# Optimization experiments

Hardware: AMD Instinct MI355X
Metric: run time of the kernel (lower is better)

## Reference

```python
import jax, jax.numpy as jnp
import numpy as np

N_NODES = 100000
N_EDGES = 1600000
IN_DIM = 128
HID = 64
OUT_DIM = 64


def setup_inputs() -> dict:
    key = jax.random.key(0)
    k = jax.random.split(key, 6)
    x = jax.random.normal(k[0], (N_NODES, IN_DIM), dtype=jnp.float32)
    edge_index = jax.random.randint(k[1], (2, N_EDGES), 0, N_NODES, dtype=jnp.int32)
    W_lin = jax.random.normal(k[2], (HID, IN_DIM), dtype=jnp.float32) * (1.0 / np.sqrt(IN_DIM))
    att = jax.random.uniform(k[3], (2 * HID,), dtype=jnp.float32, minval=-0.1, maxval=0.1)
    W_out = jax.random.normal(k[4], (OUT_DIM, HID), dtype=jnp.float32) * (1.0 / np.sqrt(HID))
    b_out = jax.random.normal(k[5], (OUT_DIM,), dtype=jnp.float32) * 0.01
    return {"x": x, "edge_index": edge_index, "W_lin": W_lin, "att": att, "W_out": W_out, "b_out": b_out}


def reference(x, edge_index, W_lin, att, W_out, b_out):
    n = x.shape[0]
    hid = W_lin.shape[0]
    h = x @ W_lin.T                                   # [N, H]
    # cat([hs,hd])*att summed == (h@a_src)[src] + (h@a_dst)[dst]
    s_node = h @ att[:hid]                            # [N]
    d_node = h @ att[hid:]                            # [N]
    src, dst = edge_index[0], edge_index[1]
    e = jax.nn.leaky_relu(s_node[src] + d_node[dst], negative_slope=0.2)  # [E]
    exp_e = jnp.exp(e - jnp.max(e))                   # global-max stabilized, as in source
    denom = jax.ops.segment_sum(exp_e, dst, num_segments=n)               # [N]
    alpha = exp_e / (denom[dst] + 1e-9)               # [E]
    msg = h[src] * alpha[:, None]                     # [E, H]
    agg = jax.ops.segment_sum(msg, dst, num_segments=n)                   # [N, H]
    z = jax.nn.relu(agg)                              # dropout is identity in eval
    return z @ W_out.T + b_out
```

## Files before the change

### kernel.cpp

```cpp
#include <hip/hip_runtime.h>

#define N_NODES 100000
#define N_EDGES 1600000
#define IN_DIM 128
#define HID 64
#define OUT_DIM 64

typedef __attribute__((ext_vector_type(8))) short short8;
typedef __attribute__((ext_vector_type(4))) float f32x4;
union FragU { short8 v; unsigned u[4]; };

__device__ __forceinline__ unsigned bf16r(float f) {
    unsigned u = __float_as_uint(f);
    return (u + 0x7FFFu + ((u >> 16) & 1u)) >> 16;
}
__device__ __forceinline__ float blo(unsigned u) { return __uint_as_float(u << 16); }
__device__ __forceinline__ float bhi(unsigned u) { return __uint_as_float(u & 0xFFFF0000u); }

#define K1_BLOCKS 1563
#define NB 782
#define CAP 2432
#define P1_BLOCKS 391
#define P1_EPB 4096
#define GRID_TOTAL (K1_BLOCKS + P1_BLOCKS)

__global__ __launch_bounds__(256) void k1_p1(const float* __restrict__ x,
                                             const float* __restrict__ W,
                                             const float* __restrict__ att,
                                             uint4* __restrict__ h4,
                                             float* __restrict__ s,
                                             float* __restrict__ d,
                                             const int* __restrict__ ei,
                                             int* __restrict__ gcount,
                                             unsigned* __restrict__ ibuf) {
    __shared__ float wsL[IN_DIM], wdL[IN_DIM];
    __shared__ __align__(16) unsigned char shmem[4 * 64 * 17 * 4];
    const int tid = threadIdx.x;
    const int bx = blockIdx.x;
    const bool is_p1 = ((bx % 5) == 4) || (bx == GRID_TOTAL - 1);

    if (is_p1) {
        int* cnt  = (int*)shmem;
        int* base = cnt + NB;
        const int blk = (bx == GRID_TOTAL - 1) ? (P1_BLOCKS - 1) : (bx / 5);
        const int e4base = blk * (P1_EPB / 4);
        for (int i = tid; i < NB; i += 256) cnt[i] = 0;
        __syncthreads();
        int pk[4][4];
#pragma unroll
        for (int c = 0; c < 4; ++c) {
            int i4 = e4base + c * 256 + tid;
            if (i4 < N_EDGES / 4) {
                int4 dv = ((const int4*)(ei + N_EDGES))[i4];
                pk[c][0] = dv.x | (atomicAdd(&cnt[dv.x >> 7], 1) << 17);
                pk[c][1] = dv.y | (atomicAdd(&cnt[dv.y >> 7], 1) << 17);
                pk[c][2] = dv.z | (atomicAdd(&cnt[dv.z >> 7], 1) << 17);
                pk[c][3] = dv.w | (atomicAdd(&cnt[dv.w >> 7], 1) << 17);
            }
        }
        __syncthreads();
        for (int b = tid; b < NB; b += 256) {
            int c = cnt[b];
            base[b] = c ? atomicAdd(&gcount[b], c) : 0;
        }
        __syncthreads();
#pragma unroll
        for (int c = 0; c < 4; ++c) {
            int i4 = e4base + c * 256 + tid;
            if (i4 < N_EDGES / 4) {
                int4 sv = ((const int4*)ei)[i4];
                int srcs[4] = {sv.x, sv.y, sv.z, sv.w};
#pragma unroll
                for (int j = 0; j < 4; ++j) {
                    unsigned p   = (unsigned)pk[c][j];
                    unsigned dst = p & 0x1FFFFu;
                    unsigned r   = p >> 17;
                    unsigned bk  = dst >> 7;
                    ibuf[bk * CAP + (unsigned)base[bk] + r] =
                        (unsigned)srcs[j] | ((dst & 127u) << 20);
                }
            }
        }
        return;
    }
    const int kb = bx - (bx + 1) / 5;

    uint4* wlds = (uint4*)shmem;
    if (tid < IN_DIM) {
        float as = 0.f, ad = 0.f;
#pragma unroll
        for (int c = 0; c < HID; ++c) {
            float w = W[c * IN_DIM + tid];
            as += w * att[c];
            ad += w * att[HID + c];
        }
        wsL[tid] = as; wdL[tid] = ad;
    }
    for (int i = tid; i < 1024; i += 256) {
        int ln = i & 63, ks = (i >> 6) & 3, t = i >> 8;
        int fl16 = ln & 15, fq = ln >> 4;
        const float* wp = &W[(t * 16 + fl16) * IN_DIM + ks * 32 + fq * 8];
        float4 wa = *(const float4*)wp;
        float4 wb = *(const float4*)(wp + 4);
        uint4 o;
        o.x = bf16r(wa.x) | (bf16r(wa.y) << 16);
        o.y = bf16r(wa.z) | (bf16r(wa.w) << 16);
        o.z = bf16r(wb.x) | (bf16r(wb.y) << 16);
        o.w = bf16r(wb.z) | (bf16r(wb.w) << 16);
        wlds[i] = o;
    }
    __syncthreads();

    const int lane = tid & 63;
    const int wv = tid >> 6;
    const int l16 = lane & 15;
    const int quad = lane >> 4;
    const int tile = kb * 4 + wv;
    const bool valid = (tile < N_NODES / 16);
    const int rowbase = tile * 16;

    f32x4 acc[4] = {{0.f,0.f,0.f,0.f},{0.f,0.f,0.f,0.f},
                    {0.f,0.f,0.f,0.f},{0.f,0.f,0.f,0.f}};
    float ps = 0.f, pd = 0.f;
    if (valid) {
        const float* xrow = &x[(size_t)(rowbase + l16) * IN_DIM];
#pragma unroll
        for (int ks = 0; ks < 4; ++ks) {
            const int k0 = ks * 32 + quad * 8;
            float4 xa = *(const float4*)&xrow[k0];
            float4 xb = *(const float4*)&xrow[k0 + 4];
            ps += xa.x * wsL[k0]     + xa.y * wsL[k0 + 1]
                + xa.z * wsL[k0 + 2] + xa.w * wsL[k0 + 3]
                + xb.x * wsL[k0 + 4] + xb.y * wsL[k0 + 5]
                + xb.z * wsL[k0 + 6] + xb.w * wsL[k0 + 7];
            pd += xa.x * wdL[k0]     + xa.y * wdL[k0 + 1]
                + xa.z * wdL[k0 + 2] + xa.w * wdL[k0 + 3]
                + xb.x * wdL[k0 + 4] + xb.y * wdL[k0 + 5]
                + xb.z * wdL[k0 + 6] + xb.w * wdL[k0 + 7];
            FragU af;
            af.u[0] = bf16r(xa.x) | (bf16r(xa.y) << 16);
            af.u[1] = bf16r(xa.z) | (bf16r(xa.w) << 16);
            af.u[2] = bf16r(xb.x) | (bf16r(xb.y) << 16);
            af.u[3] = bf16r(xb.z) | (bf16r(xb.w) << 16);
#pragma unroll
            for (int t = 0; t < 4; ++t) {
                FragU bf;
                *(uint4*)&bf = wlds[(t * 4 + ks) * 64 + lane];
                acc[t] = __builtin_amdgcn_mfma_f32_16x16x32_bf16(
                    af.v, bf.v, acc[t], 0, 0, 0);
            }
        }
        ps += __shfl_xor(ps, 16, 64); ps += __shfl_xor(ps, 32, 64);
        pd += __shfl_xor(pd, 16, 64); pd += __shfl_xor(pd, 32, 64);
        if (quad == 0) { s[rowbase + l16] = ps; d[rowbase + l16] = pd; }
    }
    __syncthreads();

    if (valid) {
        float* sc = (float*)shmem + wv * 64 * 17;
#pragma unroll
        for (int t = 0; t < 4; ++t)
#pragma unroll
            for (int r = 0; r < 4; ++r)
                sc[(l16 + 16 * t) * 17 + quad * 4 + r] = acc[t][r];
#pragma unroll
        for (int i = 0; i < 2; ++i) {
            int idx = i * 64 + lane;
            int nrow = idx >> 3, q = idx & 7;
            float v0 = sc[(q * 8 + 0) * 17 + nrow];
            float v1 = sc[(q * 8 + 1) * 17 + nrow];
            float v2 = sc[(q * 8 + 2) * 17 + nrow];
            float v3 = sc[(q * 8 + 3) * 17 + nrow];
            float v4 = sc[(q * 8 + 4) * 17 + nrow];
            float v5 = sc[(q * 8 + 5) * 17 + nrow];
            float v6 = sc[(q * 8 + 6) * 17 + nrow];
            float v7 = sc[(q * 8 + 7) * 17 + nrow];
            uint4 o;
            o.x = bf16r(v0) | (bf16r(v1) << 16);
            o.y = bf16r(v2) | (bf16r(v3) << 16);
            o.z = bf16r(v4) | (bf16r(v5) << 16);
            o.w = bf16r(v6) | (bf16r(v7) << 16);
            h4[(size_t)(rowbase + nrow) * 8 + q] = o;
        }
    }
}

__global__ __launch_bounds__(512) void k_sort_agg(const unsigned* __restrict__ ibuf,
                                                  const int* __restrict__ gcount,
                                                  const float* __restrict__ s,
                                                  const float* __restrict__ d,
                                                  const uint4* __restrict__ h4,
                                                  uint4* __restrict__ zp) {
    __shared__ uint2 el[CAP];
    __shared__ int cnt2[128], off2[128];
    __shared__ float dloc[128];
    __shared__ int wred[2];
    const int tid  = threadIdx.x;
    const int lane = tid & 63;
    const int wv   = tid >> 6;
    const int b    = blockIdx.x;

    if (tid < 128) {
        cnt2[tid] = 0;
        int dn = b * 128 + tid;
        dloc[tid] = (dn < N_NODES) ? d[dn] : 0.f;
    }
    __syncthreads();
    const int count = gcount[b];

    unsigned vk[5];
    int rk_[5];
#pragma unroll
    for (int ki = 0; ki < 5; ++ki) {
        int k = tid + ki * 512;
        vk[ki] = 0u; rk_[ki] = -1;
        if (k < count) {
            unsigned v = ibuf[(size_t)b * CAP + k];
            int dl = (int)(v >> 20);
            rk_[ki] = atomicAdd(&cnt2[dl], 1);
            vk[ki] = v;
        }
    }
    __syncthreads();

    int v0 = 0, sc0 = 0;
    if (tid < 128) {
        v0 = cnt2[tid];
        sc0 = v0;
#pragma unroll
        for (int off = 1; off < 64; off <<= 1) {
            int t = __shfl_up(sc0, off, 64);
            if (lane >= off) sc0 += t;
        }
        if (lane == 63) wred[wv] = sc0;
    }
    __syncthreads();
    if (tid < 128) {
        int excl = sc0 - v0 + ((wv == 1) ? wred[0] : 0);
        off2[tid] = excl;
    }
    __syncthreads();

#pragma unroll
    for (int ki = 0; ki < 5; ++ki) {
        if (rk_[ki] >= 0) {
            unsigned v = vk[ki];
            unsigned src = v & 0xFFFFFu;
            int dl = (int)(v >> 20);
            float e = s[src] + dloc[dl];
            e = (e > 0.f) ? e : 0.2f * e;
            float ex = __expf(e);
            el[off2[dl] + rk_[ki]] = make_uint2(src, __float_as_uint(ex));
        }
    }
    __syncthreads();

    const int l8 = tid & 7;
    const int g = tid >> 3;
#pragma unroll
    for (int half = 0; half < 2; ++half) {
        const int dl = g + half * 64;
        const int node = b * 128 + dl;
        if (node < N_NODES) {
            const int o = off2[dl];
            const int n = cnt2[dl];
            float a0 = 0.f, a1 = 0.f, a2 = 0.f, a3 = 0.f;
            float a4 = 0.f, a5 = 0.f, a6 = 0.f, a7 = 0.f, se = 0.f;
            int j = 0;
            for (; j + 7 < n; j += 8) {
                uint2 r0 = el[o + j];
                uint2 r1 = el[o + j + 1];
                uint2 r2 = el[o + j + 2];
                uint2 r3 = el[o + j + 3];
                uint2 r4 = el[o + j + 4];
                uint2 r5 = el[o + j + 5];
                uint2 r6 = el[o + j + 6];
                uint2 r7 = el[o + j + 7];
                uint4 g0 = h4[(size_t)r0.x * 8u + l8];
                uint4 g1 = h4[(size_t)r1.x * 8u + l8];
                uint4 g2 = h4[(size_t)r2.x * 8u + l8];
                uint4 g3 = h4[(size_t)r3.x * 8u + l8];
                uint4 g4 = h4[(size_t)r4.x * 8u + l8];
                uint4 g5 = h4[(size_t)r5.x * 8u + l8];
                uint4 g6 = h4[(size_t)r6.x * 8u + l8];
                uint4 g7 = h4[(size_t)r7.x * 8u + l8];
                float e0 = __uint_as_float(r0.y), e1 = __uint_as_float(r1.y);
                float e2 = __uint_as_float(r2.y), e3 = __uint_as_float(r3.y);
                float e4 = __uint_as_float(r4.y), e5 = __uint_as_float(r5.y);
                float e6 = __uint_as_float(r6.y), e7 = __uint_as_float(r7.y);
                se += ((e0 + e1) + (e2 + e3)) + ((e4 + e5) + (e6 + e7));
                a0 += e0 * blo(g0.x) + e1 * blo(g1.x) + e2 * blo(g2.x) + e3 * blo(g3.x)
                    + e4 * blo(g4.x) + e5 * blo(g5.x) + e6 * blo(g6.x) + e7 * blo(g7.x);
                a1 += e0 * bhi(g0.x) + e1 * bhi(g1.x) + e2 * bhi(g2.x) + e3 * bhi(g3.x)
                    + e4 * bhi(g4.x) + e5 * bhi(g5.x) + e6 * bhi(g6.x) + e7 * bhi(g7.x);
                a2 += e0 * blo(g0.y) + e1 * blo(g1.y) + e2 * blo(g2.y) + e3 * blo(g3.y)
                    + e4 * blo(g4.y) + e5 * blo(g5.y) + e6 * blo(g6.y) + e7 * blo(g7.y);
                a3 += e0 * bhi(g0.y) + e1 * bhi(g1.y) + e2 * bhi(g2.y) + e3 * bhi(g3.y)
                    + e4 * bhi(g4.y) + e5 * bhi(g5.y) + e6 * bhi(g6.y) + e7 * bhi(g7.y);
                a4 += e0 * blo(g0.z) + e1 * blo(g1.z) + e2 * blo(g2.z) + e3 * blo(g3.z)
                    + e4 * blo(g4.z) + e5 * blo(g5.z) + e6 * blo(g6.z) + e7 * blo(g7.z);
                a5 += e0 * bhi(g0.z) + e1 * bhi(g1.z) + e2 * bhi(g2.z) + e3 * bhi(g3.z)
                    + e4 * bhi(g4.z) + e5 * bhi(g5.z) + e6 * bhi(g6.z) + e7 * bhi(g7.z);
                a6 += e0 * blo(g0.w) + e1 * blo(g1.w) + e2 * blo(g2.w) + e3 * blo(g3.w)
                    + e4 * blo(g4.w) + e5 * blo(g5.w) + e6 * blo(g6.w) + e7 * blo(g7.w);
                a7 += e0 * bhi(g0.w) + e1 * bhi(g1.w) + e2 * bhi(g2.w) + e3 * bhi(g3.w)
                    + e4 * bhi(g4.w) + e5 * bhi(g5.w) + e6 * bhi(g6.w) + e7 * bhi(g7.w);
            }
            if (j + 3 < n) {
                uint2 r0 = el[o + j];
                uint2 r1 = el[o + j + 1];
                uint2 r2 = el[o + j + 2];
                uint2 r3 = el[o + j + 3];
                uint4 g0 = h4[(size_t)r0.x * 8u + l8];
                uint4 g1 = h4[(size_t)r1.x * 8u + l8];
                uint4 g2 = h4[(size_t)r2.x * 8u + l8];
                uint4 g3 = h4[(size_t)r3.x * 8u + l8];
                float e0 = __uint_as_float(r0.y), e1 = __uint_as_float(r1.y);
                float e2 = __uint_as_float(r2.y), e3 = __uint_as_float(r3.y);
                se += (e0 + e1) + (e2 + e3);
                a0 += e0 * blo(g0.x) + e1 * blo(g1.x) + e2 * blo(g2.x) + e3 * blo(g3.x);
                a1 += e0 * bhi(g0.x) + e1 * bhi(g1.x) + e2 * bhi(g2.x) + e3 * bhi(g3.x);
                a2 += e0 * blo(g0.y) + e1 * blo(g1.y) + e2 * blo(g2.y) + e3 * blo(g3.y);
                a3 += e0 * bhi(g0.y) + e1 * bhi(g1.y) + e2 * bhi(g2.y) + e3 * bhi(g3.y);
                a4 += e0 * blo(g0.z) + e1 * blo(g1.z) + e2 * blo(g2.z) + e3 * blo(g3.z);
                a5 += e0 * bhi(g0.z) + e1 * bhi(g1.z) + e2 * bhi(g2.z) + e3 * bhi(g3.z);
                a6 += e0 * blo(g0.w) + e1 * blo(g1.w) + e2 * blo(g2.w) + e3 * blo(g3.w);
                a7 += e0 * bhi(g0.w) + e1 * bhi(g1.w) + e2 * bhi(g2.w) + e3 * bhi(g3.w);
                j += 4;
            }
            for (; j < n; ++j) {
                uint2 r = el[o + j];
                uint4 gg = h4[(size_t)r.x * 8u + l8];
                float e = __uint_as_float(r.y);
                se += e;
                a0 += e * blo(gg.x); a1 += e * bhi(gg.x);
                a2 += e * blo(gg.y); a3 += e * bhi(gg.y);
                a4 += e * blo(gg.z); a5 += e * bhi(gg.z);
                a6 += e * blo(gg.w); a7 += e * bhi(gg.w);
            }
            float inv = 1.f / (se + 1e-9f);
            uint4 o4;
            o4.x = bf16r(fmaxf(a0 * inv, 0.f)) | (bf16r(fmaxf(a1 * inv, 0.f)) << 16);
            o4.y = bf16r(fmaxf(a2 * inv, 0.f)) | (bf16r(fmaxf(a3 * inv, 0.f)) << 16);
            o4.z = bf16r(fmaxf(a4 * inv, 0.f)) | (bf16r(fmaxf(a5 * inv, 0.f)) << 16);
            o4.w = bf16r(fmaxf(a6 * inv, 0.f)) | (bf16r(fmaxf(a7 * inv, 0.f)) << 16);
            zp[(size_t)node * 8 + l8] = o4;
        }
    }
}

#define K4_M 128
#define ZPAD 132
#define WPAD4 68

__global__ __launch_bounds__(256) void k4_out(const uint2* __restrict__ zp2,
                                              const float* __restrict__ W_out,
                                              const float* __restrict__ b_out,
                                              float* __restrict__ out) {
    __shared__ float zsT[HID * ZPAD];
    __shared__ float wsT[HID * WPAD4];
    const int tid = threadIdx.x;
    const int m0g = blockIdx.x * K4_M;
    for (int i = tid; i < OUT_DIM * HID; i += 256) {
        int c = i >> 6, k = i & 63;
        wsT[k * WPAD4 + c] = W_out[i];
    }
    for (int i = tid; i < K4_M * 16; i += 256) {
        int m = i >> 4, q = i & 15;
        int row = m0g + m;
        uint2 v = (row < N_NODES) ? zp2[row * 16 + q] : make_uint2(0u, 0u);
        int kb = q * 4;
        zsT[(kb + 0) * ZPAD + m] = blo(v.x);
        zsT[(kb + 1) * ZPAD + m] = bhi(v.x);
        zsT[(kb + 2) * ZPAD + m] = blo(v.y);
        zsT[(kb + 3) * ZPAD + m] = bhi(v.y);
    }
    __syncthreads();
    const int m0 = (tid & 31) * 4;
    const int c0 = (tid >> 5) * 8;
    float acc[4][8] = {};
#pragma unroll 4
    for (int k = 0; k < HID; ++k) {
        const float4 zv = *(const float4*)&zsT[k * ZPAD + m0];
        const float4 wa = *(const float4*)&wsT[k * WPAD4 + c0];
        const float4 wb = *(const float4*)&wsT[k * WPAD4 + c0 + 4];
#pragma unroll
        for (int i2 = 0; i2 < 4; ++i2) {
            float zi = (&zv.x)[i2];
            acc[i2][0] += zi * wa.x; acc[i2][1] += zi * wa.y;
            acc[i2][2] += zi * wa.z; acc[i2][3] += zi * wa.w;
            acc[i2][4] += zi * wb.x; acc[i2][5] += zi * wb.y;
            acc[i2][6] += zi * wb.z; acc[i2][7] += zi * wb.w;
        }
    }
    const float4 b0 = *(const float4*)&b_out[c0];
    const float4 b1 = *(const float4*)&b_out[c0 + 4];
#pragma unroll
    for (int i2 = 0; i2 < 4; ++i2) {
        int row = m0g + m0 + i2;
        if (row < N_NODES) {
            *(float4*)&out[row * OUT_DIM + c0] =
                make_float4(acc[i2][0] + b0.x, acc[i2][1] + b0.y,
                            acc[i2][2] + b0.z, acc[i2][3] + b0.w);
            *(float4*)&out[row * OUT_DIM + c0 + 4] =
                make_float4(acc[i2][4] + b1.x, acc[i2][5] + b1.y,
                            acc[i2][6] + b1.z, acc[i2][7] + b1.w);
        }
    }
}

extern "C" void kernel_launch(void* const* d_in, const int* in_sizes, int n_in,
                              void* d_out, int out_size, void* d_ws, size_t ws_size,
                              hipStream_t stream) {
    const float* x     = (const float*)d_in[0];
    const int*   ei    = (const int*)d_in[1];
    const float* W_lin = (const float*)d_in[2];
    const float* att   = (const float*)d_in[3];
    const float* W_out = (const float*)d_in[4];
    const float* b_out = (const float*)d_in[5];
    float* out = (float*)d_out;

    char* ws = (char*)d_ws;
    unsigned* h2        = (unsigned*)(ws);
    float*    s         = (float*)(ws + 12800000);
    float*    d         = (float*)(ws + 13200000);
    int*      gcount    = (int*)  (ws + 13600000);
    unsigned* ibuf      = (unsigned*)(ws + 14800016);
    unsigned* zp        = (unsigned*)(ws + 27600016);

    hipMemsetAsync(gcount, 0, NB * sizeof(int), stream);

    k1_p1<<<GRID_TOTAL, 256, 0, stream>>>(
        x, W_lin, att, (uint4*)h2, s, d, ei, gcount, ibuf);
    k_sort_agg<<<NB, 512, 0, stream>>>(ibuf, gcount, s, d, (const uint4*)h2, (uint4*)zp);
    k4_out<<<(N_NODES + K4_M - 1) / K4_M, 256, 0, stream>>>(
        (const uint2*)zp, W_out, b_out, out);
}
```

Measured before the change: 198.1 us.

## Split each 128-node aggregation bucket across two 256-thread blocks

The sort-and-aggregate kernel now launches two 256-thread blocks per 128-destination bucket instead of one 512-thread block. Each block handles 64 destinations and keeps only the edges whose local index falls in its half. The prefix scan becomes a single-wavefront scan and the LDS edge list shrinks, which should let more blocks stay resident and spread work more finely. In exchange, each bucket's edge list is read twice from global memory and each thread holds twice as many candidate registers.

```diff
diff --git a/kernel.cpp b/kernel.cpp
--- a/kernel.cpp
+++ b/kernel.cpp
@@ -20,6 +20,7 @@
 #define K1_BLOCKS 1563
 #define NB 782
 #define CAP 2432
+#define CAP_H 1280
 #define P1_BLOCKS 391
 #define P1_EPB 4096
 #define GRID_TOTAL (K1_BLOCKS + P1_BLOCKS)
@@ -185,68 +186,63 @@
     }
 }
 
-__global__ __launch_bounds__(512) void k_sort_agg(const unsigned* __restrict__ ibuf,
+__global__ __launch_bounds__(256) void k_sort_agg(const unsigned* __restrict__ ibuf,
                                                   const int* __restrict__ gcount,
                                                   const float* __restrict__ s,
                                                   const float* __restrict__ d,
                                                   const uint4* __restrict__ h4,
                                                   uint4* __restrict__ zp) {
-    __shared__ uint2 el[CAP];
-    __shared__ int cnt2[128], off2[128];
-    __shared__ float dloc[128];
-    __shared__ int wred[2];
-    const int tid  = threadIdx.x;
-    const int lane = tid & 63;
-    const int wv   = tid >> 6;
-    const int b    = blockIdx.x;
-
-    if (tid < 128) {
+    __shared__ uint2 el[CAP_H];
+    __shared__ int cnt2[64], off2[64];
+    __shared__ float dloc[64];
+    const int tid    = threadIdx.x;
+    const int bucket = blockIdx.x >> 1;
+    const int halfid = blockIdx.x & 1;
+    const int nodeb  = bucket * 128 + halfid * 64;
+
+    if (tid < 64) {
         cnt2[tid] = 0;
-        int dn = b * 128 + tid;
+        int dn = nodeb + tid;
         dloc[tid] = (dn < N_NODES) ? d[dn] : 0.f;
     }
     __syncthreads();
-    const int count = gcount[b];
-
-    unsigned vk[5];
-    int rk_[5];
-#pragma unroll
-    for (int ki = 0; ki < 5; ++ki) {
-        int k = tid + ki * 512;
+    const int count = gcount[bucket];
+
+    unsigned vk[10];
+    int rk_[10];
+#pragma unroll
+    for (int ki = 0; ki < 10; ++ki) {
+        int k = tid + ki * 256;
         vk[ki] = 0u; rk_[ki] = -1;
         if (k < count) {
-            unsigned v = ibuf[(size_t)b * CAP + k];
+            unsigned v = ibuf[(size_t)bucket * CAP + k];
             int dl = (int)(v >> 20);
-            rk_[ki] = atomicAdd(&cnt2[dl], 1);
-            vk[ki] = v;
-        }
-    }
-    __syncthreads();
-
-    int v0 = 0, sc0 = 0;
-    if (tid < 128) {
-        v0 = cnt2[tid];
-        sc0 = v0;
+            if ((dl >> 6) == halfid) {
+                rk_[ki] = atomicAdd(&cnt2[dl & 63], 1);
+                vk[ki] = v;
+            }
+        }
+    }
+    __syncthreads();
+
+    if (tid < 64) {
+        int v0 = cnt2[tid];
+        int sc0 = v0;
 #pragma unroll
         for (int off = 1; off < 64; off <<= 1) {
             int t = __shfl_up(sc0, off, 64);
-            if (lane >= off) sc0 += t;
-        }
-        if (lane == 63) wred[wv] = sc0;
-    }
-    __syncthreads();
-    if (tid < 128) {
-        int excl = sc0 - v0 + ((wv == 1) ? wred[0] : 0);
-        off2[tid] = excl;
-    }
-    __syncthreads();
-
-#pragma unroll
-    for (int ki = 0; ki < 5; ++ki) {
+            if (tid >= off) sc0 += t;
+        }
+        off2[tid] = sc0 - v0;
+    }
+    __syncthreads();
+
+#pragma unroll
+    for (int ki = 0; ki < 10; ++ki) {
         if (rk_[ki] >= 0) {
             unsigned v = vk[ki];
             unsigned src = v & 0xFFFFFu;
-            int dl = (int)(v >> 20);
+            int dl = (int)(v >> 20) & 63;
             float e = s[src] + dloc[dl];
             e = (e > 0.f) ? e : 0.2f * e;
             float ex = __expf(e);
@@ -259,8 +255,8 @@
     const int g = tid >> 3;
 #pragma unroll
     for (int half = 0; half < 2; ++half) {
-        const int dl = g + half * 64;
-        const int node = b * 128 + dl;
+        const int dl = g + half * 32;
+        const int node = nodeb + dl;
         if (node < N_NODES) {
             const int o = off2[dl];
             const int n = cnt2[dl];
@@ -432,7 +428,7 @@
 
     k1_p1<<<GRID_TOTAL, 256, 0, stream>>>(
         x, W_lin, att, (uint4*)h2, s, d, ei, gcount, ibuf);
-    k_sort_agg<<<NB, 512, 0, stream>>>(ibuf, gcount, s, d, (const uint4*)h2, (uint4*)zp);
+    k_sort_agg<<<2 * NB, 256, 0, stream>>>(ibuf, gcount, s, d, (const uint4*)h2, (uint4*)zp);
     k4_out<<<(N_NODES + K4_M - 1) / K4_M, 256, 0, stream>>>(
         (const uint2*)zp, W_out, b_out, out);
 }
```

New measurement: 199.4 us. Within noise of the previous version (+0.7%).

## Fuse output projection into aggregation kernel using bf16 MFMA

Applied to the files above, without the earlier changes.

Removes the separate output-projection kernel and the global round trip of the bf16 aggregated activations. Each aggregation block stages its 128 relu'd node rows in the shared edge buffer, then computes z @ W_out^T + b_out with 16x16x32 bf16 MFMA instructions, with W_out held as register fragments. This saves one launch plus the zp write and read. In exchange it adds W_out loads and bf16 conversion per block, more register pressure, and W_out is now rounded to bf16 where it was fp32 before.

```diff
diff --git a/kernel.cpp b/kernel.cpp
--- a/kernel.cpp
+++ b/kernel.cpp
@@ -190,21 +190,46 @@
                                                   const float* __restrict__ s,
                                                   const float* __restrict__ d,
                                                   const uint4* __restrict__ h4,
-                                                  uint4* __restrict__ zp) {
-    __shared__ uint2 el[CAP];
+                                                  const float* __restrict__ W_out,
+                                                  const float* __restrict__ b_out,
+                                                  float* __restrict__ out) {
+    __shared__ __align__(16) unsigned char elbuf[CAP * 8];
+    uint2* el    = (uint2*)elbuf;
+    uint4* zloc4 = (uint4*)elbuf;
     __shared__ int cnt2[128], off2[128];
     __shared__ float dloc[128];
     __shared__ int wred[2];
     const int tid  = threadIdx.x;
     const int lane = tid & 63;
     const int wv   = tid >> 6;
+    const int l16  = lane & 15;
+    const int quad = lane >> 4;
     const int b    = blockIdx.x;
+    const int nodeb = b * 128;
 
     if (tid < 128) {
         cnt2[tid] = 0;
-        int dn = b * 128 + tid;
+        int dn = nodeb + tid;
         dloc[tid] = (dn < N_NODES) ? d[dn] : 0.f;
     }
+
+    FragU wfrag[4][2];
+#pragma unroll
+    for (int t = 0; t < 4; ++t)
+#pragma unroll
+        for (int ks = 0; ks < 2; ++ks) {
+            const float* wp = &W_out[(t * 16 + l16) * HID + ks * 32 + quad * 8];
+            float4 wa = *(const float4*)wp;
+            float4 wb = *(const float4*)(wp + 4);
+            wfrag[t][ks].u[0] = bf16r(wa.x) | (bf16r(wa.y) << 16);
+            wfrag[t][ks].u[1] = bf16r(wa.z) | (bf16r(wa.w) << 16);
+            wfrag[t][ks].u[2] = bf16r(wb.x) | (bf16r(wb.y) << 16);
+            wfrag[t][ks].u[3] = bf16r(wb.z) | (bf16r(wb.w) << 16);
+        }
+    float bias[4];
+#pragma unroll
+    for (int t = 0; t < 4; ++t) bias[t] = b_out[t * 16 + l16];
+
     __syncthreads();
     const int count = gcount[b];
 
@@ -257,10 +282,11 @@
 
     const int l8 = tid & 7;
     const int g = tid >> 3;
+    uint4 o4h[2] = {make_uint4(0,0,0,0), make_uint4(0,0,0,0)};
 #pragma unroll
     for (int half = 0; half < 2; ++half) {
         const int dl = g + half * 64;
-        const int node = b * 128 + dl;
+        const int node = nodeb + dl;
         if (node < N_NODES) {
             const int o = off2[dl];
             const int n = cnt2[dl];
@@ -339,72 +365,36 @@
                 a6 += e * blo(gg.w); a7 += e * bhi(gg.w);
             }
             float inv = 1.f / (se + 1e-9f);
-            uint4 o4;
-            o4.x = bf16r(fmaxf(a0 * inv, 0.f)) | (bf16r(fmaxf(a1 * inv, 0.f)) << 16);
-            o4.y = bf16r(fmaxf(a2 * inv, 0.f)) | (bf16r(fmaxf(a3 * inv, 0.f)) << 16);
-            o4.z = bf16r(fmaxf(a4 * inv, 0.f)) | (bf16r(fmaxf(a5 * inv, 0.f)) << 16);
-            o4.w = bf16r(fmaxf(a6 * inv, 0.f)) | (bf16r(fmaxf(a7 * inv, 0.f)) << 16);
-            zp[(size_t)node * 8 + l8] = o4;
-        }
-    }
-}
-
-#define K4_M 128
-#define ZPAD 132
-#define WPAD4 68
-
-__global__ __launch_bounds__(256) void k4_out(const uint2* __restrict__ zp2,
-                                              const float* __restrict__ W_out,
-                                              const float* __restrict__ b_out,
-                                              float* __restrict__ out) {
-    __shared__ float zsT[HID * ZPAD];
-    __shared__ float wsT[HID * WPAD4];
-    const int tid = threadIdx.x;
-    const int m0g = blockIdx.x * K4_M;
-    for (int i = tid; i < OUT_DIM * HID; i += 256) {
-        int c = i >> 6, k = i & 63;
-        wsT[k * WPAD4 + c] = W_out[i];
-    }
-    for (int i = tid; i < K4_M * 16; i += 256) {
-        int m = i >> 4, q = i & 15;
-        int row = m0g + m;
-        uint2 v = (row < N_NODES) ? zp2[row * 16 + q] : make_uint2(0u, 0u);
-        int kb = q * 4;
-        zsT[(kb + 0) * ZPAD + m] = blo(v.x);
-        zsT[(kb + 1) * ZPAD + m] = bhi(v.x);
-        zsT[(kb + 2) * ZPAD + m] = blo(v.y);
-        zsT[(kb + 3) * ZPAD + m] = bhi(v.y);
-    }
-    __syncthreads();
-    const int m0 = (tid & 31) * 4;
-    const int c0 = (tid >> 5) * 8;
-    float acc[4][8] = {};
-#pragma unroll 4
-    for (int k = 0; k < HID; ++k) {
-        const float4 zv = *(const float4*)&zsT[k * ZPAD + m0];
-        const float4 wa = *(const float4*)&wsT[k * WPAD4 + c0];
-        const float4 wb = *(const float4*)&wsT[k * WPAD4 + c0 + 4];
-#pragma unroll
-        for (int i2 = 0; i2 < 4; ++i2) {
-            float zi = (&zv.x)[i2];
-            acc[i2][0] += zi * wa.x; acc[i2][1] += zi * wa.y;
-            acc[i2][2] += zi * wa.z; acc[i2][3] += zi * wa.w;
-            acc[i2][4] += zi * wb.x; acc[i2][5] += zi * wb.y;
-            acc[i2][6] += zi * wb.z; acc[i2][7] += zi * wb.w;
-        }
-    }
-    const float4 b0 = *(const float4*)&b_out[c0];
-    const float4 b1 = *(const float4*)&b_out[c0 + 4];
-#pragma unroll
-    for (int i2 = 0; i2 < 4; ++i2) {
-        int row = m0g + m0 + i2;
-        if (row < N_NODES) {
-            *(float4*)&out[row * OUT_DIM + c0] =
-                make_float4(acc[i2][0] + b0.x, acc[i2][1] + b0.y,
-                            acc[i2][2] + b0.z, acc[i2][3] + b0.w);
-            *(float4*)&out[row * OUT_DIM + c0 + 4] =
-                make_float4(acc[i2][4] + b1.x, acc[i2][5] + b1.y,
-                            acc[i2][6] + b1.z, acc[i2][7] + b1.w);
+            o4h[half].x = bf16r(fmaxf(a0 * inv, 0.f)) | (bf16r(fmaxf(a1 * inv, 0.f)) << 16);
+            o4h[half].y = bf16r(fmaxf(a2 * inv, 0.f)) | (bf16r(fmaxf(a3 * inv, 0.f)) << 16);
+            o4h[half].z = bf16r(fmaxf(a4 * inv, 0.f)) | (bf16r(fmaxf(a5 * inv, 0.f)) << 16);
+            o4h[half].w = bf16r(fmaxf(a6 * inv, 0.f)) | (bf16r(fmaxf(a7 * inv, 0.f)) << 16);
+        }
+    }
+    __syncthreads();
+
+    zloc4[(size_t)g * 9 + l8] = o4h[0];
+    zloc4[(size_t)(g + 64) * 9 + l8] = o4h[1];
+    __syncthreads();
+
+    f32x4 oacc[4] = {{0.f,0.f,0.f,0.f},{0.f,0.f,0.f,0.f},
+                     {0.f,0.f,0.f,0.f},{0.f,0.f,0.f,0.f}};
+#pragma unroll
+    for (int ks = 0; ks < 2; ++ks) {
+        FragU za;
+        *(uint4*)&za = zloc4[(wv * 16 + l16) * 9 + ks * 4 + quad];
+#pragma unroll
+        for (int t = 0; t < 4; ++t)
+            oacc[t] = __builtin_amdgcn_mfma_f32_16x16x32_bf16(
+                za.v, wfrag[t][ks].v, oacc[t], 0, 0, 0);
+    }
+#pragma unroll
+    for (int t = 0; t < 4; ++t) {
+#pragma unroll
+        for (int r = 0; r < 4; ++r) {
+            int node = nodeb + wv * 16 + quad * 4 + r;
+            if (node < N_NODES)
+                out[(size_t)node * OUT_DIM + t * 16 + l16] = oacc[t][r] + bias[t];
         }
     }
 }
@@ -426,13 +416,11 @@
     float*    d         = (float*)(ws + 13200000);
     int*      gcount    = (int*)  (ws + 13600000);
     unsigned* ibuf      = (unsigned*)(ws + 14800016);
-    unsigned* zp        = (unsigned*)(ws + 27600016);
 
     hipMemsetAsync(gcount, 0, NB * sizeof(int), stream);
 
     k1_p1<<<GRID_TOTAL, 256, 0, stream>>>(
         x, W_lin, att, (uint4*)h2, s, d, ei, gcount, ibuf);
-    k_sort_agg<<<NB, 512, 0, stream>>>(ibuf, gcount, s, d, (const uint4*)h2, (uint4*)zp);
-    k4_out<<<(N_NODES + K4_M - 1) / K4_M, 256, 0, stream>>>(
-        (const uint2*)zp, W_out, b_out, out);
+    k_sort_agg<<<NB, 512, 0, stream>>>(ibuf, gcount, s, d, (const uint4*)h2,
+                                       W_out, b_out, out);
 }
```

New measurement: 203.1 us. 2.5% more time.
